# Kernel optimization log

Hardware: AMD Instinct MI355X
Metric: run time of the kernel (lower is better)

## Reference

```python
import jax, jax.numpy as jnp
import numpy as np

B, S, D, H, DK = 4, 1024, 1024, 16, 64  # batch, seq (nq=nk=max_seq_len), d_model, heads, d_kqv
NEG = -1e9
BERN_P = 0.3


def setup_inputs() -> dict:
    key = jax.random.key(0)
    ks = jax.random.split(key, 12)
    xavier = lambda k, fi, fo: jax.random.uniform(k, (fi, fo), minval=-1.0, maxval=1.0) * np.sqrt(6.0 / (fi + fo))
    return {
        "x": jax.random.normal(ks[0], (B, S, D), dtype=jnp.float32),
        "mask": jax.random.randint(ks[1], (B, S), 0, 2).astype(bool),
        "pos_att": jax.random.normal(ks[2], (B, S, S), dtype=jnp.float32),
        "decoder_mask": 1,
        "Wq": xavier(ks[3], D, H * DK), "bq": jnp.zeros((H * DK,), jnp.float32),
        "Wk": xavier(ks[4], D, H * DK), "bk": jnp.zeros((H * DK,), jnp.float32),
        "Wv": xavier(ks[5], D, H * DK), "bv": jnp.zeros((H * DK,), jnp.float32),
        "Wo": xavier(ks[6], H * DK, D), "bo": jnp.zeros((D,), jnp.float32),
    }


def _forward(x, pos_att, Wq, bq, Wk, bk, Wv, bv, Wo, bo, mask, decoder_mask):
    b_s, nq, _ = x.shape
    nk = nq  # self-attention
    relu = jax.nn.relu
    # projections (Linear + activation), split into heads
    q = relu(x @ Wq + bq).reshape(b_s, nq, H, DK).transpose(0, 2, 1, 3)  # [b,h,q,d]
    k = relu(x @ Wk + bk).reshape(b_s, nk, H, DK).transpose(0, 2, 1, 3)  # [b,h,k,d]
    v = relu(x @ Wv + bv).reshape(b_s, nk, H, DK).transpose(0, 2, 1, 3)  # [b,h,k,d]
    att = jnp.einsum("bhqd,bhkd->bhqk", q, k) / np.sqrt(DK).astype(np.float32)
    # positional bias broadcast over heads
    att = att + pos_att[:, None, :, :]
    # bernoulli(0.3) noise: each kept score gets -1e9 added (deterministic key)
    bern = jax.random.bernoulli(jax.random.key(42), BERN_P, att.shape)
    att = att + bern.astype(att.dtype) * NEG
    # key-padding mask [b,1,1,nk]
    att = jnp.where(mask[:, None, None, :], NEG, att)
    # causal triu mask (decoder_mask=True path)
    if decoder_mask:
        tri = jnp.triu(jnp.ones((nq, nk), dtype=bool), k=1)
        att = jnp.where(tri[None, None, :, :], NEG, att)
    att = jax.nn.softmax(att, axis=-1)
    out = jnp.einsum("bhqk,bhkd->bqhd", att, v).reshape(b_s, nq, H * DK)
    out = relu(out @ Wo + bo)
    return out


def reference(x, mask, pos_att, decoder_mask, Wq, bq, Wk, bk, Wv, bv, Wo, bo):
    return _forward(x, pos_att, Wq, bq, Wk, bk, Wv, bv, Wo, bo, mask, decoder_mask)
```

## Files before the change

### kernel.cpp

```cpp
#include <hip/hip_runtime.h>
#include <hip/hip_bf16.h>

#define NEGV (-1e9f)

typedef __attribute__((ext_vector_type(4))) float f32x4;
typedef __attribute__((ext_vector_type(8))) short short8;

#define MFMA_BF16(a, b, c) __builtin_amdgcn_mfma_f32_16x16x32_bf16((a), (b), (c), 0, 0, 0)

#define GLOAD_LDS16(gsrc, ldst)                                                        \
    __builtin_amdgcn_global_load_lds(                                                  \
        (const __attribute__((address_space(1))) unsigned int*)(gsrc),                 \
        (__attribute__((address_space(3))) unsigned int*)(ldst), 16, 0, 0)

#define GLOAD_LDS4(gsrc, ldst)                                                         \
    __builtin_amdgcn_global_load_lds(                                                  \
        (const __attribute__((address_space(1))) unsigned int*)(gsrc),                 \
        (__attribute__((address_space(3))) unsigned int*)(ldst), 4, 0, 0)

__device__ __forceinline__ unsigned short f2bf(float f) {
    union { float f; unsigned u; } v; v.f = f;
    return (unsigned short)((v.u + 0x7fffu + ((v.u >> 16) & 1u)) >> 16);
}

__device__ __forceinline__ float bf2f(unsigned short u) {
    return __uint_as_float((unsigned)u << 16);
}

__device__ __forceinline__ bool bern_hit(unsigned idx) {
    const unsigned ks0 = 0u, ks1 = 42u, ks2 = 0x1BD11BDAu ^ 0u ^ 42u;
    unsigned x0 = ks0, x1 = idx + ks1;
#define TFR(r) { x0 += x1; x1 = __builtin_rotateleft32(x1, (unsigned)(r)); x1 ^= x0; }
    TFR(13) TFR(15) TFR(26) TFR(6)   x0 += ks1; x1 += ks2 + 1u;
    TFR(17) TFR(29) TFR(16) TFR(24)  x0 += ks2; x1 += ks0 + 2u;
    TFR(13) TFR(15) TFR(26) TFR(6)   x0 += ks0; x1 += ks1 + 3u;
    TFR(17) TFR(29) TFR(16) TFR(24)  x0 += ks1; x1 += ks2 + 4u;
    TFR(13) TFR(15) TFR(26) TFR(6)   x0 += ks2; x1 += ks0 + 5u;
#undef TFR
    unsigned bits = x0 ^ x1;
    float u = __uint_as_float((bits >> 9) | 0x3f800000u) - 1.0f;
    return u < 0.3f;
}

__global__ __launch_bounds__(256) void bern_kernel(const unsigned* __restrict__ dec,
                                                   unsigned long long* __restrict__ bw) {
    const int W = (blockIdx.x * 256 + threadIdx.x) >> 6;
    const int lane = threadIdx.x & 63;
    const int dm = (dec[0] != 0u) ? 1 : 0;
    for (int j = 0; j < 8; ++j) {
        const int p = W * 8 + j;
        const int bh = p >> 9;
        const int q = p & 511;
#pragma unroll
        for (int s = 0; s < 2; ++s) {
            const int qq = s ? (1023 - q) : q;
            const int row = (bh << 10) + qq;
            const int nw = dm ? ((qq >> 6) + 1) : 16;
            for (int kw = 0; kw < nw; ++kw) {
                const unsigned idx = ((unsigned)row << 10) + (unsigned)(kw << 6) + (unsigned)lane;
                const unsigned long long word = __ballot(bern_hit(idx));
                if (lane == 0) bw[(size_t)row * 16 + kw] = word;
            }
        }
    }
}

__global__ void prep_mask_kernel(const unsigned* __restrict__ mraw,
                                 int* __restrict__ mcanon) {
    __shared__ int f_gt1, f_nonfloatish, f_oddnz;
    const int t = threadIdx.x;
    if (t == 0) { f_gt1 = 0; f_nonfloatish = 0; f_oddnz = 0; }
    __syncthreads();
    unsigned w = mraw[t];
    if (w > 1u) f_gt1 = 1;
    if (w != 0u && w != 1u && w != 0x3f800000u) f_nonfloatish = 1;
    if ((t & 1) && w != 0u) f_oddnz = 1;
    __syncthreads();
    int mode;
    if (!f_gt1)              mode = f_oddnz ? 0 : 3;
    else if (!f_nonfloatish) mode = 2;
    else                     mode = 1;
    for (int i = t; i < 4096; i += 1024) {
        int v;
        if (mode == 0)      v = (int)mraw[i];
        else if (mode == 1) v = ((const unsigned char*)mraw)[i] ? 1 : 0;
        else if (mode == 2) v = (mraw[i] != 0u) ? 1 : 0;
        else                v = (mraw[2 * i] != 0u) ? 1 : 0;
        mcanon[i] = v;
    }
}

__global__ __launch_bounds__(256) void conv_x_kernel(const float* __restrict__ in,
                                                     unsigned short* __restrict__ out) {
    const int i = (blockIdx.x * 256 + threadIdx.x) * 4;
    float4 v = *reinterpret_cast<const float4*>(&in[i]);
    ushort4 o;
    o.x = f2bf(v.x); o.y = f2bf(v.y); o.z = f2bf(v.z); o.w = f2bf(v.w);
    *reinterpret_cast<ushort4*>(&out[i]) = o;
}

__global__ __launch_bounds__(256) void conv_wt_kernel(const float* __restrict__ W,
                                                      unsigned short* __restrict__ WT) {
    __shared__ float ts[64][68];
    const int t = threadIdx.x;
    const int k0 = blockIdx.y * 64, n0 = blockIdx.x * 64;
    const int r = t >> 4, c4 = (t & 15) * 4;
#pragma unroll
    for (int rr = 0; rr < 4; ++rr) {
        const int row = r + rr * 16;
        float4 v = *reinterpret_cast<const float4*>(&W[(size_t)(k0 + row) * 1024 + n0 + c4]);
        ts[row][c4 + 0] = v.x; ts[row][c4 + 1] = v.y;
        ts[row][c4 + 2] = v.z; ts[row][c4 + 3] = v.w;
    }
    __syncthreads();
#pragma unroll
    for (int rr = 0; rr < 4; ++rr) {
        const int n = r + rr * 16;
        ushort4 o;
        o.x = f2bf(ts[c4 + 0][n]); o.y = f2bf(ts[c4 + 1][n]);
        o.z = f2bf(ts[c4 + 2][n]); o.w = f2bf(ts[c4 + 3][n]);
        *reinterpret_cast<ushort4*>(&WT[(size_t)(n0 + n) * 1024 + k0 + c4]) = o;
    }
}

__global__ void concat_bias_kernel(const float* __restrict__ a, const float* __restrict__ b,
                                   const float* __restrict__ c, float* __restrict__ o) {
    const int i = blockIdx.x * 256 + threadIdx.x;
    o[i] = (i < 1024) ? a[i] : ((i < 2048) ? b[i - 1024] : c[i - 2048]);
}

template<int MF, int WMODE>
__global__ __launch_bounds__(256) void gemm_bf16(
    const unsigned short* __restrict__ A, const unsigned short* __restrict__ BT,
    const float* __restrict__ bias, void* __restrict__ Cout,
    int M, int N, int K) {
    __shared__ unsigned short As[MF * 2048];
    __shared__ unsigned short Bs[8192];
    const int t = threadIdx.x;
    const int lane = t & 63, w = t >> 6;
    const int wr = w >> 1, wc = w & 1;
    const int lgrp = lane >> 4, l15 = lane & 15;
    const int m0 = blockIdx.y * (MF * 32), n0 = blockIdx.x * 128;
    const int srow = t >> 3;
    const int scol = ((t & 7) ^ (srow & 7)) << 3;
    const int rdsw = (l15 & 7) << 4;
    f32x4 acc[MF][4] = {};

    for (int k0 = 0; k0 < K; k0 += 64) {
#pragma unroll
        for (int s = 0; s < MF; ++s)
            GLOAD_LDS16(&A[(size_t)(m0 + s * 32 + srow) * K + (k0 + scol)], &As[s * 2048 + t * 8]);
#pragma unroll
        for (int s = 0; s < 4; ++s)
            GLOAD_LDS16(&BT[(size_t)(n0 + s * 32 + srow) * K + (k0 + scol)], &Bs[s * 2048 + t * 8]);
        __syncthreads();
#pragma unroll
        for (int kkh = 0; kkh < 2; ++kkh) {
            const int klb = (kkh * 32 + (lgrp << 3)) * 2;
            short8 af[MF], bf[4];
#pragma unroll
            for (int i = 0; i < MF; ++i)
                af[i] = *(const short8*)((const char*)As + (wr * (MF * 16) + i * 16 + l15) * 128 + (klb ^ rdsw));
#pragma unroll
            for (int i = 0; i < 4; ++i)
                bf[i] = *(const short8*)((const char*)Bs + (wc * 64 + i * 16 + l15) * 128 + (klb ^ rdsw));
#pragma unroll
            for (int mf = 0; mf < MF; ++mf)
#pragma unroll
                for (int nf = 0; nf < 4; ++nf)
                    acc[mf][nf] = MFMA_BF16(af[mf], bf[nf], acc[mf][nf]);
        }
        __syncthreads();
    }
#pragma unroll
    for (int nf = 0; nf < 4; ++nf) {
        const int n = n0 + wc * 64 + nf * 16 + l15;
        const float bv = bias[n];
#pragma unroll
        for (int mf = 0; mf < MF; ++mf) {
#pragma unroll
            for (int r = 0; r < 4; ++r) {
                const int m = m0 + wr * (MF * 16) + mf * 16 + (lgrp << 2) + r;
                float v = fmaxf(acc[mf][nf][r] + bv, 0.f);
                if (WMODE == 0) {
                    ((float*)Cout)[(size_t)m * N + n] = v;
                } else if (WMODE == 1) {
                    ((unsigned short*)Cout)[(size_t)m * N + n] = f2bf(v);
                } else {
                    const int which = n >> 10;
                    ((unsigned short*)Cout)[(size_t)which * 4194304u + (size_t)m * 1024 + (n & 1023)] = f2bf(v);
                }
            }
        }
    }
}

__global__ __launch_bounds__(256) void vsum_part(const unsigned short* __restrict__ Vb,
                                                 float* __restrict__ part) {
    const int c = blockIdx.x, b = blockIdx.y, t = threadIdx.x;
    float a0 = 0, a1 = 0, a2 = 0, a3 = 0;
    const unsigned short* src = &Vb[((size_t)(b * 1024 + c * 64)) * 1024 + t * 4];
    for (int r = 0; r < 64; ++r) {
        ushort4 v = *(const ushort4*)(src + (size_t)r * 1024);
        a0 += bf2f(v.x); a1 += bf2f(v.y); a2 += bf2f(v.z); a3 += bf2f(v.w);
    }
    float4 o = {a0, a1, a2, a3};
    *(float4*)&part[(size_t)(b * 16 + c) * 1024 + t * 4] = o;
}

__global__ __launch_bounds__(256) void vsum_reduce(const float* __restrict__ part,
                                                   float* __restrict__ vmean) {
    const int b = blockIdx.x, t = threadIdx.x;
    float4 s = {0, 0, 0, 0};
    for (int c = 0; c < 16; ++c) {
        float4 v = *(const float4*)&part[(size_t)(b * 16 + c) * 1024 + t * 4];
        s.x += v.x; s.y += v.y; s.z += v.z; s.w += v.w;
    }
    const float sc = 1.0f / 1024.0f;
    float4 o = {s.x * sc, s.y * sc, s.z * sc, s.w * sc};
    *(float4*)&vmean[b * 1024 + t * 4] = o;
}

__global__ __launch_bounds__(256) void attn_kernel(
    const unsigned short* __restrict__ Qb, const unsigned short* __restrict__ Kb,
    const unsigned short* __restrict__ Vb, const float* __restrict__ pos,
    const int* __restrict__ mcanon, const unsigned* __restrict__ dec,
    const unsigned long long* __restrict__ bern, const float* __restrict__ vmean,
    unsigned short* __restrict__ AO) {
    const int gx = blockIdx.x, h = blockIdx.y, b = blockIdx.z;
    const int t = threadIdx.x, lane = t & 63, w = t >> 6;
    const int lgrp = lane >> 4, l15 = lane & 15;

    __shared__ unsigned short Ks[4096];
    __shared__ unsigned short VT[4096];
    __shared__ float pos_s[4096];
    __shared__ int mask_s[64];

    const int dm = (dec[0] != 0u) ? 1 : 0;
    const int qt = (int)((0x765489AB3210CDEFull >> (((gx + 4 * b) & 15) << 2)) & 15);
    const int q0 = qt * 64;
    const int ntiles = dm ? (qt + 1) : 16;
    const int qi = q0 + w * 16 + l15;

    const size_t qg = ((size_t)(b * 1024 + qi)) * 1024 + h * 64 + (lgrp << 3);
    const short8 qb0 = *(const short8*)&Qb[qg];
    const short8 qb1 = *(const short8*)&Qb[qg + 32];
    const unsigned browbase = ((unsigned)((b * 16 + h) * 1024 + qi)) * 16u;

    float m = -3e38f, l = 0.f;
    f32x4 osc[4] = {};
    const int qor = w * 16 + (lgrp << 2);

    for (int kt = 0; kt < ntiles; ++kt) {
        const int kbase = kt * 64;
        {
            const int srow = t >> 3;
            const int scol = ((t & 7) ^ (srow & 7)) << 3;
            GLOAD_LDS16(&Kb[((size_t)(b * 1024 + kbase + srow)) * 1024 + h * 64 + scol],
                        &Ks[t * 8]);
            GLOAD_LDS16(&Kb[((size_t)(b * 1024 + kbase + 32 + srow)) * 1024 + h * 64 + scol],
                        &Ks[2048 + t * 8]);
        }
#pragma unroll
        for (int s = 0; s < 4; ++s) {
            const int row = w * 16 + s * 4 + (lane >> 4);
            const int scol = ((lane & 15) ^ (row & 15)) << 2;
            GLOAD_LDS16(&pos[((size_t)(b * 1024 + q0 + row)) * 1024 + kbase + scol],
                        &pos_s[w * 1024 + s * 256 + lane * 4]);
        }
        if (w == 0) GLOAD_LDS4(&mcanon[b * 1024 + kbase + lane], &mask_s[lane]);
        const unsigned long long bwv = bern[browbase + kt];
        {
            const int p = t >> 3;
            const int dblk = (t & 7) << 3;
            const unsigned short* vs = &Vb[((size_t)(b * 1024 + kbase + 2 * p)) * 1024 + h * 64 + dblk];
            short8 v0 = *(const short8*)vs;
            short8 v1 = *(const short8*)(vs + 1024);
#pragma unroll
            for (int j = 0; j < 8; ++j) {
                const int d = dblk + j;
                const int sw = (d & 7) ^ ((d >> 3) & 7);
                unsigned word = (unsigned)(unsigned short)v0[j] |
                                ((unsigned)(unsigned short)v1[j] << 16);
                *(unsigned*)((char*)VT + d * 128 + ((((2 * p) >> 3) ^ sw) << 4) +
                             (((2 * p) & 7) << 1)) = word;
            }
        }
        __syncthreads();

        f32x4 sacc[4] = {};
#pragma unroll
        for (int kkh = 0; kkh < 2; ++kkh) {
            const int klb = (kkh * 32 + (lgrp << 3)) * 2;
            const short8 qf = kkh ? qb1 : qb0;
#pragma unroll
            for (int f = 0; f < 4; ++f) {
                short8 kf = *(const short8*)((const char*)Ks + (f * 16 + l15) * 128 +
                                             (klb ^ ((l15 & 7) << 4)));
                sacc[f] = MFMA_BF16(kf, qf, sacc[f]);
            }
        }

        float p16[4][4];
        float tmax = -3e38f;
#pragma unroll
        for (int f = 0; f < 4; ++f) {
            const f32x4 posq = *(const f32x4*)&pos_s[(w * 16 + l15) * 64 +
                                                     (((f * 4 + lgrp) ^ l15) << 2)];
            const int4 mq = *(const int4*)&mask_s[f * 16 + (lgrp << 2)];
            const int mqa[4] = {mq.x, mq.y, mq.z, mq.w};
            const unsigned nib = (unsigned)(bwv >> (f * 16 + (lgrp << 2))) & 0xFu;
#pragma unroll
            for (int r = 0; r < 4; ++r) {
                const int ki = kbase + f * 16 + (lgrp << 2) + r;
                float lg = NEGV;
                const bool live = (mqa[r] == 0) && !(dm && (ki > qi));
                if (live) {
                    float sc = fmaf(sacc[f][r], 0.125f, posq[r]);
                    sc += ((nib >> r) & 1u) ? NEGV : 0.f;
                    lg = sc;
                }
                p16[f][r] = lg;
                tmax = fmaxf(tmax, lg);
            }
        }
        tmax = fmaxf(tmax, __shfl_xor(tmax, 16, 64));
        tmax = fmaxf(tmax, __shfl_xor(tmax, 32, 64));
        const float mn = fmaxf(m, tmax);
        const float fac = __expf(m - mn);

        float psum = 0.f;
        unsigned pk[4][2];
#pragma unroll
        for (int f = 0; f < 4; ++f) {
#pragma unroll
            for (int rr = 0; rr < 2; ++rr) {
                float pa = __expf(p16[f][2 * rr] - mn);
                float pb = __expf(p16[f][2 * rr + 1] - mn);
                psum += pa + pb;
                pk[f][rr] = (unsigned)f2bf(pa) | ((unsigned)f2bf(pb) << 16);
            }
        }
        psum += __shfl_xor(psum, 16, 64);
        psum += __shfl_xor(psum, 32, 64);
        l = l * fac + psum;
        m = mn;

#pragma unroll
        for (int r = 0; r < 4; ++r) {
            const float fr = __int_as_float(__builtin_amdgcn_ds_bpermute(
                (((lgrp << 2) + r) << 2), __float_as_int(fac)));
#pragma unroll
            for (int nf = 0; nf < 4; ++nf) osc[nf][r] *= fr;
        }

        {
            const int idx0 = ((((lgrp << 1) & 3) << 4) | l15) << 2;
            const int idx1 = (((((lgrp << 1) + 1) & 3) << 4) | l15) << 2;
            const bool hi = (lgrp >> 1) != 0;
#pragma unroll
            for (int kkh = 0; kkh < 2; ++kkh) {
                union { unsigned u[4]; short8 s; } pa;
#pragma unroll
                for (int s2 = 0; s2 < 4; ++s2) {
                    const int rr = s2 & 1;
                    const int idx = (s2 >> 1) ? idx1 : idx0;
                    const unsigned lo = (unsigned)__builtin_amdgcn_ds_bpermute(idx, (int)pk[kkh * 2][rr]);
                    const unsigned hw = (unsigned)__builtin_amdgcn_ds_bpermute(idx, (int)pk[kkh * 2 + 1][rr]);
                    pa.u[s2] = hi ? hw : lo;
                }
#pragma unroll
                for (int nf = 0; nf < 4; ++nf) {
                    const int d = nf * 16 + l15;
                    const int sw = (d & 7) ^ ((d >> 3) & 7);
                    short8 vf = *(const short8*)((const char*)VT + d * 128 +
                                                 ((((kkh << 2) + lgrp) ^ sw) << 4));
                    osc[nf] = MFMA_BF16(pa.s, vf, osc[nf]);
                }
            }
        }
        __syncthreads();
    }

#pragma unroll
    for (int r = 0; r < 4; ++r) {
        const int src = (((lgrp << 2) + r) << 2);
        const float lr = __int_as_float(__builtin_amdgcn_ds_bpermute(src, __float_as_int(l)));
        const float mr = __int_as_float(__builtin_amdgcn_ds_bpermute(src, __float_as_int(m)));
        const int qo = q0 + qor + r;
        const bool dgen = (mr == NEGV);
        const float inv = 1.0f / lr;
#pragma unroll
        for (int nf = 0; nf < 4; ++nf) {
            const int d = nf * 16 + l15;
            float v = dgen ? vmean[b * 1024 + h * 64 + d] : osc[nf][r] * inv;
            AO[((size_t)(b * 1024 + qo)) * 1024 + h * 64 + d] = f2bf(v);
        }
    }
}

extern "C" void kernel_launch(void* const* d_in, const int* in_sizes, int n_in,
                              void* d_out, int out_size, void* d_ws, size_t ws_size,
                              hipStream_t stream) {
    const float* x       = (const float*)d_in[0];
    const unsigned* mraw = (const unsigned*)d_in[1];
    const float* pos     = (const float*)d_in[2];
    const unsigned* dec  = (const unsigned*)d_in[3];
    const float* Wq = (const float*)d_in[4];  const float* bq = (const float*)d_in[5];
    const float* Wk = (const float*)d_in[6];  const float* bk = (const float*)d_in[7];
    const float* Wv = (const float*)d_in[8];  const float* bv = (const float*)d_in[9];
    const float* Wo = (const float*)d_in[10]; const float* bo = (const float*)d_in[11];
    float* out = (float*)d_out;

    char* ws = (char*)d_ws;
    unsigned short* xb   = (unsigned short*)(ws);
    unsigned short* wcat = (unsigned short*)(ws + (8u << 20));
    unsigned short* wto  = wcat + 3u * 1024 * 1024;
    float* bcat          = (float*)(ws + (16u << 20));
    int* mcanon          = (int*)(ws + (16u << 20) + (64u << 10));
    unsigned short* Qb   = (unsigned short*)(ws + (17u << 20));
    unsigned short* Kb   = Qb + 4u * 1024 * 1024;
    unsigned short* Vb   = Qb + 8u * 1024 * 1024;
    unsigned short* AO   = (unsigned short*)(ws + (41u << 20));
    unsigned long long* bern = (unsigned long long*)(ws + (49u << 20));
    float* part  = (float*)(ws);
    float* vmean = (float*)(ws + (1u << 19));

    prep_mask_kernel<<<1, 1024, 0, stream>>>(mraw, mcanon);
    bern_kernel<<<1024, 256, 0, stream>>>(dec, bern);
    conv_x_kernel<<<4096, 256, 0, stream>>>(x, xb);
    dim3 tg(16, 16);
    conv_wt_kernel<<<tg, 256, 0, stream>>>(Wq, wcat);
    conv_wt_kernel<<<tg, 256, 0, stream>>>(Wk, wcat + 1024u * 1024u);
    conv_wt_kernel<<<tg, 256, 0, stream>>>(Wv, wcat + 2u * 1024u * 1024u);
    conv_wt_kernel<<<tg, 256, 0, stream>>>(Wo, wto);
    concat_bias_kernel<<<12, 256, 0, stream>>>(bq, bk, bv, bcat);

    gemm_bf16<4, 2><<<dim3(24, 32), 256, 0, stream>>>(xb, wcat, bcat, Qb, 4096, 3072, 1024);

    vsum_part<<<dim3(16, 4), 256, 0, stream>>>(Vb, part);
    vsum_reduce<<<4, 256, 0, stream>>>(part, vmean);

    attn_kernel<<<dim3(16, 16, 4), 256, 0, stream>>>(Qb, Kb, Vb, pos, mcanon, dec, bern, vmean, AO);

    gemm_bf16<2, 0><<<dim3(8, 64), 256, 0, stream>>>(AO, wto, bo, out, 4096, 1024, 1024);
}
```

Before: 340.5 us.

## Fuse Bernoulli mask generation into QKV GEMM launch via interleaved block roles

Result: no change. 338.7 us (-0.5%).

```diff
diff --git a/kernel.cpp b/kernel.cpp
--- a/kernel.cpp
+++ b/kernel.cpp
@@ -27,43 +27,21 @@
     return __uint_as_float((unsigned)u << 16);
 }
 
-__device__ __forceinline__ bool bern_hit(unsigned idx) {
+#define ROTL(x, r) __builtin_amdgcn_alignbit((x), (x), 32 - (r))
+
+__device__ __forceinline__ unsigned tf_bits(unsigned idx) {
     const unsigned ks0 = 0u, ks1 = 42u, ks2 = 0x1BD11BDAu ^ 0u ^ 42u;
     unsigned x0 = ks0, x1 = idx + ks1;
-#define TFR(r) { x0 += x1; x1 = __builtin_rotateleft32(x1, (unsigned)(r)); x1 ^= x0; }
+#define TFR(r) { x0 += x1; x1 = ROTL(x1, (r)); x1 ^= x0; }
     TFR(13) TFR(15) TFR(26) TFR(6)   x0 += ks1; x1 += ks2 + 1u;
     TFR(17) TFR(29) TFR(16) TFR(24)  x0 += ks2; x1 += ks0 + 2u;
     TFR(13) TFR(15) TFR(26) TFR(6)   x0 += ks0; x1 += ks1 + 3u;
     TFR(17) TFR(29) TFR(16) TFR(24)  x0 += ks1; x1 += ks2 + 4u;
     TFR(13) TFR(15) TFR(26) TFR(6)   x0 += ks2; x1 += ks0 + 5u;
 #undef TFR
-    unsigned bits = x0 ^ x1;
-    float u = __uint_as_float((bits >> 9) | 0x3f800000u) - 1.0f;
-    return u < 0.3f;
-}
-
-__global__ __launch_bounds__(256) void bern_kernel(const unsigned* __restrict__ dec,
-                                                   unsigned long long* __restrict__ bw) {
-    const int W = (blockIdx.x * 256 + threadIdx.x) >> 6;
-    const int lane = threadIdx.x & 63;
-    const int dm = (dec[0] != 0u) ? 1 : 0;
-    for (int j = 0; j < 8; ++j) {
-        const int p = W * 8 + j;
-        const int bh = p >> 9;
-        const int q = p & 511;
-#pragma unroll
-        for (int s = 0; s < 2; ++s) {
-            const int qq = s ? (1023 - q) : q;
-            const int row = (bh << 10) + qq;
-            const int nw = dm ? ((qq >> 6) + 1) : 16;
-            for (int kw = 0; kw < nw; ++kw) {
-                const unsigned idx = ((unsigned)row << 10) + (unsigned)(kw << 6) + (unsigned)lane;
-                const unsigned long long word = __ballot(bern_hit(idx));
-                if (lane == 0) bw[(size_t)row * 16 + kw] = word;
-            }
-        }
-    }
-}
+    return x0 ^ x1;
+}
+#define BERN_THRESH 1288490496u
 
 __global__ void prep_mask_kernel(const unsigned* __restrict__ mraw,
                                  int* __restrict__ mcanon) {
@@ -129,6 +107,103 @@
     o[i] = (i < 1024) ? a[i] : ((i < 2048) ? b[i - 1024] : c[i - 2048]);
 }
 
+__global__ __launch_bounds__(256) void qkv_bern_kernel(
+    const unsigned short* __restrict__ A, const unsigned short* __restrict__ BT,
+    const float* __restrict__ bias, unsigned short* __restrict__ Cout,
+    const unsigned* __restrict__ dec, unsigned long long* __restrict__ bw) {
+    __shared__ unsigned short As[8192];
+    __shared__ unsigned short Bs[8192];
+    const int bid = blockIdx.x;
+    const int grp = bid / 7, res = bid % 7;
+    const int t = threadIdx.x;
+
+    if (!(res & 1) || res == 0 ? (res == 0 || res == 2 || res == 4) : false) {}
+    if (res == 0 || res == 2 || res == 4) {
+        const int g = grp * 3 + (res >> 1);
+        const int lane = t & 63, w = t >> 6;
+        const int wr = w >> 1, wc = w & 1;
+        const int lgrp = lane >> 4, l15 = lane & 15;
+        const int m0 = (g / 24) * 128, n0 = (g % 24) * 128;
+        const int srow = t >> 3;
+        const int scol = ((t & 7) ^ (srow & 7)) << 3;
+        const int rdsw = (l15 & 7) << 4;
+        f32x4 acc[4][4] = {};
+
+        for (int k0 = 0; k0 < 1024; k0 += 64) {
+#pragma unroll
+            for (int s = 0; s < 4; ++s)
+                GLOAD_LDS16(&A[(size_t)(m0 + s * 32 + srow) * 1024 + (k0 + scol)], &As[s * 2048 + t * 8]);
+#pragma unroll
+            for (int s = 0; s < 4; ++s)
+                GLOAD_LDS16(&BT[(size_t)(n0 + s * 32 + srow) * 1024 + (k0 + scol)], &Bs[s * 2048 + t * 8]);
+            __syncthreads();
+#pragma unroll
+            for (int kkh = 0; kkh < 2; ++kkh) {
+                const int klb = (kkh * 32 + (lgrp << 3)) * 2;
+                short8 af[4], bf[4];
+#pragma unroll
+                for (int i = 0; i < 4; ++i) {
+                    af[i] = *(const short8*)((const char*)As + (wr * 64 + i * 16 + l15) * 128 + (klb ^ rdsw));
+                    bf[i] = *(const short8*)((const char*)Bs + (wc * 64 + i * 16 + l15) * 128 + (klb ^ rdsw));
+                }
+#pragma unroll
+                for (int mf = 0; mf < 4; ++mf)
+#pragma unroll
+                    for (int nf = 0; nf < 4; ++nf)
+                        acc[mf][nf] = MFMA_BF16(af[mf], bf[nf], acc[mf][nf]);
+            }
+            __syncthreads();
+        }
+#pragma unroll
+        for (int nf = 0; nf < 4; ++nf) {
+            const int n = n0 + wc * 64 + nf * 16 + l15;
+            const float bv = bias[n];
+#pragma unroll
+            for (int mf = 0; mf < 4; ++mf) {
+#pragma unroll
+                for (int r = 0; r < 4; ++r) {
+                    const int m = m0 + wr * 64 + mf * 16 + (lgrp << 2) + r;
+                    float v = fmaxf(acc[mf][nf][r] + bv, 0.f);
+                    const int which = n >> 10;
+                    Cout[(size_t)which * 4194304u + (size_t)m * 1024 + (n & 1023)] = f2bf(v);
+                }
+            }
+        }
+    } else {
+        static const int bmap[7] = {0, 0, 0, 1, 0, 2, 3};
+        const int W = (grp * 4 + bmap[res]) * 4 + (t >> 6);
+        const int lane = t & 63;
+        const int dm = (dec[0] != 0u) ? 1 : 0;
+        for (int j = 0; j < 8; ++j) {
+            const int p = W * 8 + j;
+            const int bh = p >> 9;
+            const int q = p & 511;
+            const int row0 = (bh << 10) + q;
+            const int row1 = (bh << 10) + 1023 - q;
+            const int nw0 = dm ? ((q >> 6) + 1) : 16;
+            const int nw1 = dm ? (16 - (q >> 6)) : 16;
+            const unsigned b0 = ((unsigned)row0 << 10) + (unsigned)lane;
+            const unsigned b1 = ((unsigned)row1 << 10) + (unsigned)lane;
+            int kw = 0;
+            for (; kw < nw0; ++kw) {
+                const unsigned bits0 = tf_bits(b0 + (unsigned)(kw << 6));
+                const unsigned bits1 = tf_bits(b1 + (unsigned)(kw << 6));
+                const unsigned long long w0 = __ballot(bits0 < BERN_THRESH);
+                const unsigned long long w1 = __ballot(bits1 < BERN_THRESH);
+                if (lane == 0) {
+                    bw[(size_t)row0 * 16 + kw] = w0;
+                    bw[(size_t)row1 * 16 + kw] = w1;
+                }
+            }
+            for (; kw < nw1; ++kw) {
+                const unsigned bits1 = tf_bits(b1 + (unsigned)(kw << 6));
+                const unsigned long long w1 = __ballot(bits1 < BERN_THRESH);
+                if (lane == 0) bw[(size_t)row1 * 16 + kw] = w1;
+            }
+        }
+    }
+}
+
 template<int MF, int WMODE>
 __global__ __launch_bounds__(256) void gemm_bf16(
     const unsigned short* __restrict__ A, const unsigned short* __restrict__ BT,
@@ -184,11 +259,8 @@
                 float v = fmaxf(acc[mf][nf][r] + bv, 0.f);
                 if (WMODE == 0) {
                     ((float*)Cout)[(size_t)m * N + n] = v;
-                } else if (WMODE == 1) {
+                } else {
                     ((unsigned short*)Cout)[(size_t)m * N + n] = f2bf(v);
-                } else {
-                    const int which = n >> 10;
-                    ((unsigned short*)Cout)[(size_t)which * 4194304u + (size_t)m * 1024 + (n & 1023)] = f2bf(v);
                 }
             }
         }
@@ -427,7 +499,6 @@
     float* vmean = (float*)(ws + (1u << 19));
 
     prep_mask_kernel<<<1, 1024, 0, stream>>>(mraw, mcanon);
-    bern_kernel<<<1024, 256, 0, stream>>>(dec, bern);
     conv_x_kernel<<<4096, 256, 0, stream>>>(x, xb);
     dim3 tg(16, 16);
     conv_wt_kernel<<<tg, 256, 0, stream>>>(Wq, wcat);
@@ -436,7 +507,7 @@
     conv_wt_kernel<<<tg, 256, 0, stream>>>(Wo, wto);
     concat_bias_kernel<<<12, 256, 0, stream>>>(bq, bk, bv, bcat);
 
-    gemm_bf16<4, 2><<<dim3(24, 32), 256, 0, stream>>>(xb, wcat, bcat, Qb, 4096, 3072, 1024);
+    qkv_bern_kernel<<<1792, 256, 0, stream>>>(xb, wcat, bcat, Qb, dec, bern);
 
     vsum_part<<<dim3(16, 4), 256, 0, stream>>>(Vb, part);
     vsum_reduce<<<4, 256, 0, stream>>>(part, vmean);
```

## Fuse preprocessing and Bernoulli mask generation into one interleaved kernel; add MFMA priority hints

Applied to the files above, without the earlier changes.

After: 348.9 us. 1.02x slower.

```diff
diff --git a/kernel.cpp b/kernel.cpp
--- a/kernel.cpp
+++ b/kernel.cpp
@@ -27,106 +27,135 @@
     return __uint_as_float((unsigned)u << 16);
 }
 
-__device__ __forceinline__ bool bern_hit(unsigned idx) {
+#define ROTL(x, r) __builtin_amdgcn_alignbit((x), (x), 32 - (r))
+
+__device__ __forceinline__ unsigned tf_bits(unsigned idx) {
     const unsigned ks0 = 0u, ks1 = 42u, ks2 = 0x1BD11BDAu ^ 0u ^ 42u;
     unsigned x0 = ks0, x1 = idx + ks1;
-#define TFR(r) { x0 += x1; x1 = __builtin_rotateleft32(x1, (unsigned)(r)); x1 ^= x0; }
+#define TFR(r) { x0 += x1; x1 = ROTL(x1, (r)); x1 ^= x0; }
     TFR(13) TFR(15) TFR(26) TFR(6)   x0 += ks1; x1 += ks2 + 1u;
     TFR(17) TFR(29) TFR(16) TFR(24)  x0 += ks2; x1 += ks0 + 2u;
     TFR(13) TFR(15) TFR(26) TFR(6)   x0 += ks0; x1 += ks1 + 3u;
     TFR(17) TFR(29) TFR(16) TFR(24)  x0 += ks1; x1 += ks2 + 4u;
     TFR(13) TFR(15) TFR(26) TFR(6)   x0 += ks2; x1 += ks0 + 5u;
 #undef TFR
-    unsigned bits = x0 ^ x1;
-    float u = __uint_as_float((bits >> 9) | 0x3f800000u) - 1.0f;
-    return u < 0.3f;
-}
-
-__global__ __launch_bounds__(256) void bern_kernel(const unsigned* __restrict__ dec,
-                                                   unsigned long long* __restrict__ bw) {
-    const int W = (blockIdx.x * 256 + threadIdx.x) >> 6;
-    const int lane = threadIdx.x & 63;
-    const int dm = (dec[0] != 0u) ? 1 : 0;
-    for (int j = 0; j < 8; ++j) {
-        const int p = W * 8 + j;
-        const int bh = p >> 9;
-        const int q = p & 511;
-#pragma unroll
-        for (int s = 0; s < 2; ++s) {
-            const int qq = s ? (1023 - q) : q;
-            const int row = (bh << 10) + qq;
-            const int nw = dm ? ((qq >> 6) + 1) : 16;
-            for (int kw = 0; kw < nw; ++kw) {
-                const unsigned idx = ((unsigned)row << 10) + (unsigned)(kw << 6) + (unsigned)lane;
-                const unsigned long long word = __ballot(bern_hit(idx));
-                if (lane == 0) bw[(size_t)row * 16 + kw] = word;
-            }
-        }
-    }
-}
-
-__global__ void prep_mask_kernel(const unsigned* __restrict__ mraw,
-                                 int* __restrict__ mcanon) {
-    __shared__ int f_gt1, f_nonfloatish, f_oddnz;
+    return x0 ^ x1;
+}
+#define BERN_THRESH 1288490496u
+
+__global__ __launch_bounds__(256) void prep_bern_kernel(
+    const float* __restrict__ x,
+    const float* __restrict__ Wq, const float* __restrict__ Wk,
+    const float* __restrict__ Wv, const float* __restrict__ Wo,
+    const float* __restrict__ bq, const float* __restrict__ bk,
+    const float* __restrict__ bv,
+    const unsigned* __restrict__ mraw, const unsigned* __restrict__ dec,
+    unsigned short* __restrict__ xb, unsigned short* __restrict__ wcat,
+    unsigned short* __restrict__ wto, float* __restrict__ bcat,
+    int* __restrict__ mcanon, unsigned long long* __restrict__ bw) {
+    __shared__ float ts[64][68];
+    __shared__ int fl_gt1, fl_nf, fl_odz;
+    const int bid = blockIdx.x;
     const int t = threadIdx.x;
-    if (t == 0) { f_gt1 = 0; f_nonfloatish = 0; f_oddnz = 0; }
-    __syncthreads();
-    unsigned w = mraw[t];
-    if (w > 1u) f_gt1 = 1;
-    if (w != 0u && w != 1u && w != 0x3f800000u) f_nonfloatish = 1;
-    if ((t & 1) && w != 0u) f_oddnz = 1;
-    __syncthreads();
-    int mode;
-    if (!f_gt1)              mode = f_oddnz ? 0 : 3;
-    else if (!f_nonfloatish) mode = 2;
-    else                     mode = 1;
-    for (int i = t; i < 4096; i += 1024) {
-        int v;
-        if (mode == 0)      v = (int)mraw[i];
-        else if (mode == 1) v = ((const unsigned char*)mraw)[i] ? 1 : 0;
-        else if (mode == 2) v = (mraw[i] != 0u) ? 1 : 0;
-        else                v = (mraw[2 * i] != 0u) ? 1 : 0;
-        mcanon[i] = v;
-    }
-}
-
-__global__ __launch_bounds__(256) void conv_x_kernel(const float* __restrict__ in,
-                                                     unsigned short* __restrict__ out) {
-    const int i = (blockIdx.x * 256 + threadIdx.x) * 4;
-    float4 v = *reinterpret_cast<const float4*>(&in[i]);
-    ushort4 o;
-    o.x = f2bf(v.x); o.y = f2bf(v.y); o.z = f2bf(v.z); o.w = f2bf(v.w);
-    *reinterpret_cast<ushort4*>(&out[i]) = o;
-}
-
-__global__ __launch_bounds__(256) void conv_wt_kernel(const float* __restrict__ W,
-                                                      unsigned short* __restrict__ WT) {
-    __shared__ float ts[64][68];
-    const int t = threadIdx.x;
-    const int k0 = blockIdx.y * 64, n0 = blockIdx.x * 64;
-    const int r = t >> 4, c4 = (t & 15) * 4;
-#pragma unroll
-    for (int rr = 0; rr < 4; ++rr) {
-        const int row = r + rr * 16;
-        float4 v = *reinterpret_cast<const float4*>(&W[(size_t)(k0 + row) * 1024 + n0 + c4]);
-        ts[row][c4 + 0] = v.x; ts[row][c4 + 1] = v.y;
-        ts[row][c4 + 2] = v.z; ts[row][c4 + 3] = v.w;
-    }
-    __syncthreads();
-#pragma unroll
-    for (int rr = 0; rr < 4; ++rr) {
-        const int n = r + rr * 16;
-        ushort4 o;
-        o.x = f2bf(ts[c4 + 0][n]); o.y = f2bf(ts[c4 + 1][n]);
-        o.z = f2bf(ts[c4 + 2][n]); o.w = f2bf(ts[c4 + 3][n]);
-        *reinterpret_cast<ushort4*>(&WT[(size_t)(n0 + n) * 1024 + k0 + c4]) = o;
-    }
-}
-
-__global__ void concat_bias_kernel(const float* __restrict__ a, const float* __restrict__ b,
-                                   const float* __restrict__ c, float* __restrict__ o) {
-    const int i = blockIdx.x * 256 + threadIdx.x;
-    o[i] = (i < 1024) ? a[i] : ((i < 2048) ? b[i - 1024] : c[i - 2048]);
+
+    if (bid & 1) {
+        const int dm = (dec[0] != 0u) ? 1 : 0;
+        const int wgid = ((bid >> 1) << 2) + (t >> 6);
+        const int lane = t & 63;
+        const int G = dm ? 139264 : 262144;
+        for (int g = wgid; g < G; g += 6144) {
+            int f = __builtin_amdgcn_readfirstlane(g) << 2;
+            int kw;
+            if (dm) {
+                kw = 0;
+                while (f >= ((16 - kw) << 12)) { f -= (16 - kw) << 12; ++kw; }
+            } else {
+                kw = f >> 16; f &= 65535;
+            }
+            const int qoff = f >> 6;
+            const int bh0 = f & 63;
+            const int q = (dm ? (kw << 6) : 0) + qoff;
+            const unsigned base = ((unsigned)q << 10) + ((unsigned)kw << 6) + (unsigned)lane;
+            const unsigned i0 = base + ((unsigned)(bh0 + 0) << 20);
+            const unsigned i1 = base + ((unsigned)(bh0 + 1) << 20);
+            const unsigned i2 = base + ((unsigned)(bh0 + 2) << 20);
+            const unsigned i3 = base + ((unsigned)(bh0 + 3) << 20);
+            const unsigned r0 = tf_bits(i0), r1 = tf_bits(i1);
+            const unsigned r2 = tf_bits(i2), r3 = tf_bits(i3);
+            const unsigned long long w0 = __ballot(r0 < BERN_THRESH);
+            const unsigned long long w1 = __ballot(r1 < BERN_THRESH);
+            const unsigned long long w2 = __ballot(r2 < BERN_THRESH);
+            const unsigned long long w3 = __ballot(r3 < BERN_THRESH);
+            if (lane == 0) {
+                const size_t rb = ((size_t)(((bh0 << 10) + q) << 4)) + (size_t)kw;
+                bw[rb]         = w0;
+                bw[rb + 16384] = w1;
+                bw[rb + 32768] = w2;
+                bw[rb + 49152] = w3;
+            }
+        }
+    } else {
+        const int idx = bid >> 1;
+        if (idx < 1024) {
+            const int which = idx >> 8, tile = idx & 255;
+            const float* W = (which == 0) ? Wq : (which == 1) ? Wk : (which == 2) ? Wv : Wo;
+            unsigned short* WT = (which < 3) ? (wcat + (size_t)which * 1048576u) : wto;
+            const int k0 = (tile >> 4) * 64, n0 = (tile & 15) * 64;
+            const int r = t >> 4, c4 = (t & 15) * 4;
+#pragma unroll
+            for (int rr = 0; rr < 4; ++rr) {
+                const int row = r + rr * 16;
+                float4 v = *reinterpret_cast<const float4*>(&W[(size_t)(k0 + row) * 1024 + n0 + c4]);
+                ts[row][c4 + 0] = v.x; ts[row][c4 + 1] = v.y;
+                ts[row][c4 + 2] = v.z; ts[row][c4 + 3] = v.w;
+            }
+            __syncthreads();
+#pragma unroll
+            for (int rr = 0; rr < 4; ++rr) {
+                const int n = r + rr * 16;
+                ushort4 o;
+                o.x = f2bf(ts[c4 + 0][n]); o.y = f2bf(ts[c4 + 1][n]);
+                o.z = f2bf(ts[c4 + 2][n]); o.w = f2bf(ts[c4 + 3][n]);
+                *reinterpret_cast<ushort4*>(&WT[(size_t)(n0 + n) * 1024 + k0 + c4]) = o;
+            }
+        } else if (idx < 1536) {
+            const int c = idx - 1024;
+            const float* src = x + (size_t)c * 8192;
+            unsigned short* dst = xb + (size_t)c * 8192;
+#pragma unroll
+            for (int j = 0; j < 8; ++j) {
+                const int off = j * 1024 + t * 4;
+                float4 v = *reinterpret_cast<const float4*>(src + off);
+                ushort4 o;
+                o.x = f2bf(v.x); o.y = f2bf(v.y); o.z = f2bf(v.z); o.w = f2bf(v.w);
+                *reinterpret_cast<ushort4*>(dst + off) = o;
+            }
+        } else {
+            if (t == 0) { fl_gt1 = 0; fl_nf = 0; fl_odz = 0; }
+            __syncthreads();
+            for (int i = t; i < 1024; i += 256) {
+                unsigned w0 = mraw[i];
+                if (w0 > 1u) fl_gt1 = 1;
+                if (w0 != 0u && w0 != 1u && w0 != 0x3f800000u) fl_nf = 1;
+                if ((i & 1) && w0 != 0u) fl_odz = 1;
+            }
+            __syncthreads();
+            int mode;
+            if (!fl_gt1)      mode = fl_odz ? 0 : 3;
+            else if (!fl_nf)  mode = 2;
+            else              mode = 1;
+            for (int i = t; i < 4096; i += 256) {
+                int v;
+                if (mode == 0)      v = (int)mraw[i];
+                else if (mode == 1) v = ((const unsigned char*)mraw)[i] ? 1 : 0;
+                else if (mode == 2) v = (mraw[i] != 0u) ? 1 : 0;
+                else                v = (mraw[2 * i] != 0u) ? 1 : 0;
+                mcanon[i] = v;
+            }
+            for (int i = t; i < 3072; i += 256)
+                bcat[i] = (i < 1024) ? bq[i] : ((i < 2048) ? bk[i - 1024] : bv[i - 2048]);
+        }
+    }
 }
 
 template<int MF, int WMODE>
@@ -164,11 +193,13 @@
 #pragma unroll
             for (int i = 0; i < 4; ++i)
                 bf[i] = *(const short8*)((const char*)Bs + (wc * 64 + i * 16 + l15) * 128 + (klb ^ rdsw));
+            __builtin_amdgcn_s_setprio(1);
 #pragma unroll
             for (int mf = 0; mf < MF; ++mf)
 #pragma unroll
                 for (int nf = 0; nf < 4; ++nf)
                     acc[mf][nf] = MFMA_BF16(af[mf], bf[nf], acc[mf][nf]);
+            __builtin_amdgcn_s_setprio(0);
         }
         __syncthreads();
     }
@@ -289,6 +320,7 @@
         __syncthreads();
 
         f32x4 sacc[4] = {};
+        __builtin_amdgcn_s_setprio(1);
 #pragma unroll
         for (int kkh = 0; kkh < 2; ++kkh) {
             const int klb = (kkh * 32 + (lgrp << 3)) * 2;
@@ -300,6 +332,7 @@
                 sacc[f] = MFMA_BF16(kf, qf, sacc[f]);
             }
         }
+        __builtin_amdgcn_s_setprio(0);
 
         float p16[4][4];
         float tmax = -3e38f;
@@ -369,6 +402,7 @@
                     const unsigned hw = (unsigned)__builtin_amdgcn_ds_bpermute(idx, (int)pk[kkh * 2 + 1][rr]);
                     pa.u[s2] = hi ? hw : lo;
                 }
+                __builtin_amdgcn_s_setprio(1);
 #pragma unroll
                 for (int nf = 0; nf < 4; ++nf) {
                     const int d = nf * 16 + l15;
@@ -377,6 +411,7 @@
                                                  ((((kkh << 2) + lgrp) ^ sw) << 4));
                     osc[nf] = MFMA_BF16(pa.s, vf, osc[nf]);
                 }
+                __builtin_amdgcn_s_setprio(0);
             }
         }
         __syncthreads();
@@ -426,15 +461,9 @@
     float* part  = (float*)(ws);
     float* vmean = (float*)(ws + (1u << 19));
 
-    prep_mask_kernel<<<1, 1024, 0, stream>>>(mraw, mcanon);
-    bern_kernel<<<1024, 256, 0, stream>>>(dec, bern);
-    conv_x_kernel<<<4096, 256, 0, stream>>>(x, xb);
-    dim3 tg(16, 16);
-    conv_wt_kernel<<<tg, 256, 0, stream>>>(Wq, wcat);
-    conv_wt_kernel<<<tg, 256, 0, stream>>>(Wk, wcat + 1024u * 1024u);
-    conv_wt_kernel<<<tg, 256, 0, stream>>>(Wv, wcat + 2u * 1024u * 1024u);
-    conv_wt_kernel<<<tg, 256, 0, stream>>>(Wo, wto);
-    concat_bias_kernel<<<12, 256, 0, stream>>>(bq, bk, bv, bcat);
+    prep_bern_kernel<<<3073, 256, 0, stream>>>(x, Wq, Wk, Wv, Wo, bq, bk, bv,
+                                               mraw, dec, xb, wcat, wto, bcat,
+                                               mcanon, bern);
 
     gemm_bf16<4, 2><<<dim3(24, 32), 256, 0, stream>>>(xb, wcat, bcat, Qb, 4096, 3072, 1024);
 
```
